# Performance work log

Measured on AMD Instinct MI355X. Metric: run time of the kernel, lower is better.

## Reference

```python
import jax, jax.numpy as jnp
import numpy as np

# dims: batch, tokens, channels, heads, head_dim, slices, context_slices, context_dim
B, N, C, H, D, G, SC, DC = 2, 32768, 256, 8, 32, 32, 64, 32
EPS_SLICE = 1e-5


def _ln(x, g, b):
    m = x.mean(-1, keepdims=True)
    v = ((x - m) ** 2).mean(-1, keepdims=True)
    return (x - m) * jax.lax.rsqrt(v + 1e-5) * g + b


def setup_inputs() -> dict:
    key = jax.random.key(0)
    ks = jax.random.split(key, 16)
    w = lambda k, s: jax.random.normal(k, s, jnp.float32) * 0.02
    return dict(
        fx=jax.random.normal(ks[0], (B, N, C), jnp.float32),
        context=jax.random.normal(ks[1], (B, H, SC, DC), jnp.float32),
        ln1_g=jnp.ones((C,), jnp.float32), ln1_b=jnp.zeros((C,), jnp.float32),
        Wfx=w(ks[2], (C, H * D)), bfx=jnp.zeros((H * D,), jnp.float32),
        Wx=w(ks[3], (C, H * D)), bx=jnp.zeros((H * D,), jnp.float32),
        Wslice=w(ks[4], (D, G)), bslice=jnp.zeros((G,), jnp.float32),
        temperature=0.5 * jnp.ones((1, H, 1, 1), jnp.float32),
        Wq=w(ks[5], (D, D)), Wk=w(ks[6], (D, D)), Wv=w(ks[7], (D, D)),
        Wcq=w(ks[8], (D, D)), bcq=jnp.zeros((D,), jnp.float32),
        Wck=w(ks[9], (DC, D)), bck=jnp.zeros((D,), jnp.float32),
        Wcv=w(ks[10], (DC, D)), bcv=jnp.zeros((D,), jnp.float32),
        state_mixing=jnp.zeros((), jnp.float32),
        Wout=w(ks[11], (H * D, C)), bout=jnp.zeros((C,), jnp.float32),
        ln2_g=jnp.ones((C,), jnp.float32), ln2_b=jnp.zeros((C,), jnp.float32),
        Wm1=w(ks[12], (C, 4 * C)), bm1=jnp.zeros((4 * C,), jnp.float32),
        Wm2=w(ks[13], (4 * C, C)), bm2=jnp.zeros((C,), jnp.float32),
    )


def reference(fx, context, ln1_g, ln1_b, Wfx, bfx, Wx, bx, Wslice, bslice,
              temperature, Wq, Wk, Wv, Wcq, bcq, Wck, bck, Wcv, bcv,
              state_mixing, Wout, bout, ln2_g, ln2_b, Wm1, bm1, Wm2, bm2):
    # --- GALE attention on pre-normed input (Transolver physics attention + cross) ---
    x = _ln(fx, ln1_g, ln1_b)
    fxm = (x @ Wfx + bfx).reshape(B, N, H, D).transpose(0, 2, 1, 3)  # b h n d
    xm = (x @ Wx + bx).reshape(B, N, H, D).transpose(0, 2, 1, 3)    # b h n d
    # slice weights: softmax over slices with learnable per-head temperature
    sw = jax.nn.softmax((xm @ Wslice + bslice) / temperature, axis=-1)  # b h n g
    norm = sw.sum(2)  # b h g
    st = jnp.einsum('bhnd,bhng->bhgd', fxm, sw) / (norm + EPS_SLICE)[..., None]
    scale = D ** -0.5
    # self-attention among slice tokens (no bias on q/k/v)
    q, k, v = st @ Wq, st @ Wk, st @ Wv
    sattn = jax.nn.softmax(jnp.einsum('bhgd,bhmd->bhgm', q, k) * scale, axis=-1)
    self_tok = jnp.einsum('bhgm,bhmd->bhgd', sattn, v)
    # cross-attention of slice tokens onto geometry/global context
    cq = st @ Wcq + bcq
    ck = context @ Wck + bck
    cv = context @ Wcv + bcv
    cattn = jax.nn.softmax(jnp.einsum('bhgd,bhsd->bhgs', cq, ck) * scale, axis=-1)
    cross_tok = jnp.einsum('bhgs,bhsd->bhgd', cattn, cv)
    # sigmoid-gated mix
    mw = jax.nn.sigmoid(state_mixing)
    ost = mw * self_tok + (1.0 - mw) * cross_tok
    # de-slice back to tokens and output-project
    out = jnp.einsum('bhgd,bhng->bhnd', ost, sw)
    out = out.transpose(0, 2, 1, 3).reshape(B, N, H * D) @ Wout + bout
    fx = fx + out  # residual 1
    # --- MLP block ---
    h = _ln(fx, ln2_g, ln2_b)
    fx = fx + (jax.nn.gelu(h @ Wm1 + bm1, approximate=False) @ Wm2 + bm2)
    return fx
```

## Files before the change

### kernel.cpp

```cpp
#include <hip/hip_runtime.h>
#include <hip/hip_bf16.h>

#define BATCH 2
#define NTOK  32768
#define CH    256
#define NH    8
#define HDIM  32
#define NG    32
#define NSC   64
#define NDC   32

typedef __attribute__((ext_vector_type(8))) short short8v;
typedef __attribute__((ext_vector_type(4))) short short4v;
typedef __attribute__((ext_vector_type(4))) float f32x4;

static __device__ __forceinline__ short f2bf(float f) {
    __hip_bfloat16 h = __float2bfloat16(f);
    return __builtin_bit_cast(short, h);
}
static __device__ __forceinline__ float bf2f(short s) {
    return __bfloat162float(__builtin_bit_cast(__hip_bfloat16, s));
}

__global__ __launch_bounds__(256) void kconv_transpose(
    const float* __restrict__ in, __hip_bfloat16* __restrict__ out,
    int K, int N)
{
    __shared__ float t[32][33];
    const int nb = N >> 5;
    const int bk = blockIdx.x / nb;
    const int bn = blockIdx.x % nb;
    const int c = threadIdx.x & 31, r0 = threadIdx.x >> 5;
    #pragma unroll
    for (int i = 0; i < 4; ++i) {
        const int r = r0 + i * 8;
        t[r][c] = in[(long)(bk * 32 + r) * N + bn * 32 + c];
    }
    __syncthreads();
    #pragma unroll
    for (int i = 0; i < 4; ++i) {
        const int r = r0 + i * 8;
        out[(long)(bn * 32 + r) * K + bk * 32 + c] = __float2bfloat16(t[c][r]);
    }
}

__global__ __launch_bounds__(256) void kcomb(
    const float* __restrict__ Wx, const float* __restrict__ bx,
    const float* __restrict__ Wsl, const float* __restrict__ bsl,
    __hip_bfloat16* __restrict__ wcat2, float* __restrict__ bcomb)
{
    __shared__ float wcol[32];
    const int hc = blockIdx.x;
    const int h = hc >> 5, g = hc & 31;
    const int tid = threadIdx.x;
    if (tid < 32) wcol[tid] = Wsl[tid * 32 + g];
    __syncthreads();
    float a = 0.f;
    #pragma unroll
    for (int d = 0; d < 32; ++d) a += Wx[tid * 256 + h * 32 + d] * wcol[d];
    wcat2[(long)hc * 256 + tid] = __float2bfloat16(a);
    if (tid == 0) {
        float s = bsl[g];
        #pragma unroll
        for (int d = 0; d < 32; ++d) s += bx[h * 32 + d] * wcol[d];
        bcomb[hc] = s;
    }
}

__global__ __launch_bounds__(256, 2) void k1_mfma(
    const float* __restrict__ fx,
    const float* __restrict__ g1, const float* __restrict__ b1,
    const __hip_bfloat16* __restrict__ wcat,
    const float* __restrict__ bfx, const float* __restrict__ bcomb,
    const float* __restrict__ temp,
    __hip_bfloat16* __restrict__ fxm_o, __hip_bfloat16* __restrict__ sw_o)
{
    __shared__ __align__(16) char lds[65536];
    const int tid = threadIdx.x;
    const int lane = tid & 63, wid = tid >> 6;
    const long tok0 = (long)blockIdx.x * 64;
    const int col = lane & 15, kq = lane >> 4;
    const int swz = (col & 7) << 4;
    const int ep = ((kq * 16) ^ swz) & 48;
    const int e0 = (swz & 64) | ep;
    const int e1 = ((swz & 64) ^ 64) | ep;
    const int ab0 = col * 512 + e0, ab1 = col * 512 + e1;

    {
        const float4 gv = *reinterpret_cast<const float4*>(g1 + lane * 4);
        const float4 bv = *reinterpret_cast<const float4*>(b1 + lane * 4);
        for (int tt = 0; tt < 16; ++tt) {
            const int r = wid * 16 + tt;
            const float4 v = *reinterpret_cast<const float4*>(fx + (tok0 + r) * 256 + lane * 4);
            float s = v.x + v.y + v.z + v.w;
            float s2 = v.x * v.x + v.y * v.y + v.z * v.z + v.w * v.w;
            #pragma unroll
            for (int off = 32; off; off >>= 1) {
                s  += __shfl_xor(s,  off);
                s2 += __shfl_xor(s2, off);
            }
            const float mean = s * (1.f / 256.f);
            const float rs = rsqrtf(s2 * (1.f / 256.f) - mean * mean + 1e-5f);
            short4v o;
            o[0] = f2bf((v.x - mean) * rs * gv.x + bv.x);
            o[1] = f2bf((v.y - mean) * rs * gv.y + bv.y);
            o[2] = f2bf((v.z - mean) * rs * gv.z + bv.z);
            o[3] = f2bf((v.w - mean) * rs * gv.w + bv.w);
            const int addr = r * 512 + ((lane * 8) ^ ((r & 7) << 4));
            *reinterpret_cast<short4v*>(lds + addr) = o;
        }
    }
    __syncthreads();

    f32x4 acc[4][8];
    #pragma unroll
    for (int mt = 0; mt < 4; ++mt)
        #pragma unroll
        for (int nt = 0; nt < 8; ++nt) acc[mt][nt] = (f32x4){0.f, 0.f, 0.f, 0.f};

    const short* wp = reinterpret_cast<const short*>(wcat) + (wid * 128 + col) * 256 + kq * 8;
    #pragma unroll 2
    for (int j = 0; j < 4; ++j) {
        short8v a0[4], a1[4];
        #pragma unroll
        for (int mt = 0; mt < 4; ++mt) {
            a0[mt] = *reinterpret_cast<const short8v*>(lds + mt * 8192 + j * 128 + ab0);
            a1[mt] = *reinterpret_cast<const short8v*>(lds + mt * 8192 + j * 128 + ab1);
        }
        #pragma unroll
        for (int nt = 0; nt < 8; ++nt) {
            const short8v b0 = *reinterpret_cast<const short8v*>(wp + nt * 4096 + j * 64);
            const short8v b1 = *reinterpret_cast<const short8v*>(wp + nt * 4096 + j * 64 + 32);
            #pragma unroll
            for (int mt = 0; mt < 4; ++mt) {
                acc[mt][nt] = __builtin_amdgcn_mfma_f32_16x16x32_bf16(a0[mt], b0, acc[mt][nt], 0, 0, 0);
                acc[mt][nt] = __builtin_amdgcn_mfma_f32_16x16x32_bf16(a1[mt], b1, acc[mt][nt], 0, 0, 0);
            }
        }
    }
    __syncthreads();

    #pragma unroll
    for (int nt = 0; nt < 8; ++nt) {
        const int c = wid * 128 + nt * 16 + col;
        const float bb = (c < 256) ? bfx[c] : bcomb[c - 256];
        #pragma unroll
        for (int mt = 0; mt < 4; ++mt) {
            #pragma unroll
            for (int r = 0; r < 4; ++r) {
                const int row = mt * 16 + kq * 4 + r;
                const int byte = row * 1024 + ((c * 2) ^ ((row & 7) << 4));
                *reinterpret_cast<short*>(lds + byte) = f2bf(acc[mt][nt][r] + bb);
            }
        }
    }
    __syncthreads();

    #pragma unroll
    for (int it = 0; it < 8; ++it) {
        const int idx = it * 256 + tid;
        const int row = idx >> 5, ch = idx & 31;
        const short8v val = *reinterpret_cast<const short8v*>(
            lds + row * 1024 + ((ch * 16) ^ ((row & 7) << 4)));
        *reinterpret_cast<short8v*>(
            reinterpret_cast<short*>(fxm_o) + (tok0 + row) * 256 + ch * 8) = val;
    }

    #pragma unroll
    for (int pp = 0; pp < 2; ++pp) {
        const int p = pp * 256 + tid;
        const int t = p >> 3, h = p & 7;
        const float it_ = 1.f / temp[h];
        float lg[32];
        #pragma unroll
        for (int g = 0; g < 32; ++g) {
            const int byte = t * 1024 + (((256 + h * 32 + g) * 2) ^ ((t & 7) << 4));
            lg[g] = bf2f(*reinterpret_cast<const short*>(lds + byte)) * it_;
        }
        float mx = -1e30f;
        #pragma unroll
        for (int g = 0; g < 32; ++g) mx = fmaxf(mx, lg[g]);
        float ssum = 0.f;
        #pragma unroll
        for (int g = 0; g < 32; ++g) { lg[g] = __expf(lg[g] - mx); ssum += lg[g]; }
        const float inv = 1.f / ssum;
        #pragma unroll
        for (int g = 0; g < 32; ++g) {
            const int byte = t * 1024 + (((256 + h * 32 + g) * 2) ^ ((t & 7) << 4));
            *reinterpret_cast<short*>(lds + byte) = f2bf(lg[g] * inv);
        }
    }
    __syncthreads();

    #pragma unroll
    for (int it = 0; it < 8; ++it) {
        const int idx = it * 256 + tid;
        const int row = idx >> 5, ch = idx & 31;
        const short8v val = *reinterpret_cast<const short8v*>(
            lds + row * 1024 + ((512 + ch * 16) ^ ((row & 7) << 4)));
        *reinterpret_cast<short8v*>(
            reinterpret_cast<short*>(sw_o) + (tok0 + row) * 256 + ch * 8) = val;
    }
}

__global__ __launch_bounds__(256) void k2_st_partial(
    const __hip_bfloat16* __restrict__ fxm, const __hip_bfloat16* __restrict__ sw,
    float* __restrict__ pst, float* __restrict__ pn)
{
    __shared__ float psum[4][32][32];
    __shared__ float pns[4][32];
    const int tid = threadIdx.x, wid = tid >> 6, lane = tid & 63;
    const int blk = blockIdx.x;
    const int bh = blk >> 5, chunk = blk & 31;
    const int b = bh >> 3, h = bh & 7;
    const long rbase = (long)b * NTOK + (long)chunk * 1024 + wid * 256;
    const int gB = lane >> 3, dB = lane & 7;
    const short* sp = reinterpret_cast<const short*>(sw) + rbase * 256 + h * 32 + gB * 4;
    const short* fp = reinterpret_cast<const short*>(fxm) + rbase * 256 + h * 32 + dB * 4;

    float acc[4][4];
    float nacc[4];
    #pragma unroll
    for (int i = 0; i < 4; ++i) {
        nacc[i] = 0.f;
        #pragma unroll
        for (int j = 0; j < 4; ++j) acc[i][j] = 0.f;
    }

    #pragma unroll 4
    for (int r = 0; r < 256; ++r) {
        const short4v s4 = *reinterpret_cast<const short4v*>(sp + r * 256);
        const short4v f4 = *reinterpret_cast<const short4v*>(fp + r * 256);
        float sg[4], fd[4];
        #pragma unroll
        for (int i = 0; i < 4; ++i) { sg[i] = bf2f(s4[i]); fd[i] = bf2f(f4[i]); }
        #pragma unroll
        for (int gg = 0; gg < 4; ++gg) {
            nacc[gg] += sg[gg];
            #pragma unroll
            for (int dd = 0; dd < 4; ++dd) acc[gg][dd] += sg[gg] * fd[dd];
        }
    }

    #pragma unroll
    for (int gg = 0; gg < 4; ++gg) {
        #pragma unroll
        for (int dd = 0; dd < 4; ++dd)
            psum[wid][gB * 4 + gg][dB * 4 + dd] = acc[gg][dd];
        if (dB == 0) pns[wid][gB * 4 + gg] = nacc[gg];
    }
    __syncthreads();

    for (int i = tid; i < 1024; i += 256) {
        const int g = i >> 5, d = i & 31;
        pst[(long)blk * 1024 + i] =
            psum[0][g][d] + psum[1][g][d] + psum[2][g][d] + psum[3][g][d];
    }
    if (tid < 32)
        pn[blk * 32 + tid] = pns[0][tid] + pns[1][tid] + pns[2][tid] + pns[3][tid];
}

__global__ __launch_bounds__(256) void k3_slice_attn(
    const float* __restrict__ pst, const float* __restrict__ pn,
    const float* __restrict__ ctx,
    const float* __restrict__ Wq, const float* __restrict__ Wk, const float* __restrict__ Wv,
    const float* __restrict__ Wcq, const float* __restrict__ bcq,
    const float* __restrict__ Wck, const float* __restrict__ bck,
    const float* __restrict__ Wcv, const float* __restrict__ bcv,
    const float* __restrict__ mix, __hip_bfloat16* __restrict__ ostT_o)
{
    __shared__ float st[1024], qm[1024], km[1024], vm[1024], cqm[1024];
    __shared__ float ckm[2048], cvm[2048], attn[2048], stok[1024], nb[32];
    const int tid = threadIdx.x;
    const int bh = blockIdx.x;

    if (tid < 32) {
        float s = 0.f;
        for (int c = 0; c < 32; ++c) s += pn[(bh * 32 + c) * 32 + tid];
        nb[tid] = s;
    }
    __syncthreads();
    for (int i = tid; i < 1024; i += 256) {
        float s = 0.f;
        for (int c = 0; c < 32; ++c) s += pst[(long)(bh * 32 + c) * 1024 + i];
        st[i] = s / (nb[i >> 5] + 1e-5f);
    }
    __syncthreads();

    for (int i = tid; i < 1024; i += 256) {
        const int g = i >> 5, d = i & 31;
        float aq = 0.f, ak = 0.f, av = 0.f, ac = bcq[d];
        #pragma unroll
        for (int e = 0; e < 32; ++e) {
            const float s = st[g * 32 + e];
            aq += s * Wq[e * 32 + d];
            ak += s * Wk[e * 32 + d];
            av += s * Wv[e * 32 + d];
            ac += s * Wcq[e * 32 + d];
        }
        qm[i] = aq; km[i] = ak; vm[i] = av; cqm[i] = ac;
    }
    const float* cbp = ctx + (long)bh * (NSC * NDC);
    for (int i = tid; i < 2048; i += 256) {
        const int s_ = i >> 5, d = i & 31;
        float w1 = bck[d], w2 = bcv[d];
        #pragma unroll
        for (int e = 0; e < 32; ++e) {
            const float cval = cbp[s_ * 32 + e];
            w1 += cval * Wck[e * 32 + d];
            w2 += cval * Wcv[e * 32 + d];
        }
        ckm[i] = w1; cvm[i] = w2;
    }
    __syncthreads();

    const float scale = 0.17677669529663687f;
    for (int i = tid; i < 1024; i += 256) {
        const int g = i >> 5, m = i & 31;
        float a = 0.f;
        #pragma unroll
        for (int d = 0; d < 32; ++d) a += qm[g * 32 + d] * km[m * 32 + d];
        attn[i] = a * scale;
    }
    __syncthreads();
    if (tid < 32) {
        float mx = -1e30f;
        for (int m = 0; m < 32; ++m) mx = fmaxf(mx, attn[tid * 32 + m]);
        float s = 0.f;
        for (int m = 0; m < 32; ++m) { const float e = expf(attn[tid * 32 + m] - mx); attn[tid * 32 + m] = e; s += e; }
        const float inv = 1.f / s;
        for (int m = 0; m < 32; ++m) attn[tid * 32 + m] *= inv;
    }
    __syncthreads();
    for (int i = tid; i < 1024; i += 256) {
        const int g = i >> 5, d = i & 31;
        float a = 0.f;
        #pragma unroll
        for (int m = 0; m < 32; ++m) a += attn[g * 32 + m] * vm[m * 32 + d];
        stok[i] = a;
    }
    __syncthreads();
    for (int i = tid; i < 2048; i += 256) {
        const int g = i >> 6, s_ = i & 63;
        float a = 0.f;
        #pragma unroll
        for (int d = 0; d < 32; ++d) a += cqm[g * 32 + d] * ckm[s_ * 32 + d];
        attn[i] = a * scale;
    }
    __syncthreads();
    if (tid < 32) {
        float mx = -1e30f;
        for (int m = 0; m < 64; ++m) mx = fmaxf(mx, attn[tid * 64 + m]);
        float s = 0.f;
        for (int m = 0; m < 64; ++m) { const float e = expf(attn[tid * 64 + m] - mx); attn[tid * 64 + m] = e; s += e; }
        const float inv = 1.f / s;
        for (int m = 0; m < 64; ++m) attn[tid * 64 + m] *= inv;
    }
    __syncthreads();
    const float mw = 1.f / (1.f + expf(-mix[0]));
    for (int i = tid; i < 1024; i += 256) {
        const int g = i >> 5, d = i & 31;
        float a = 0.f;
        #pragma unroll
        for (int s_ = 0; s_ < 64; ++s_) a += attn[g * 64 + s_] * cvm[s_ * 32 + d];
        const float val = mw * stok[i] + (1.f - mw) * a;
        ostT_o[(long)bh * 1024 + d * 32 + g] = __float2bfloat16(val);
    }
}

__global__ __launch_bounds__(256, 2) void k4_mfma(
    const __hip_bfloat16* __restrict__ sw, const __hip_bfloat16* __restrict__ ostT,
    const __hip_bfloat16* __restrict__ woutt, const float* __restrict__ bout,
    const float* __restrict__ fx, float* __restrict__ out)
{
    __shared__ __align__(16) char lds[65536];
    const int tid = threadIdx.x;
    const int lane = tid & 63, wid = tid >> 6;
    const long tok0 = (long)blockIdx.x * 64;
    const int b = (int)(tok0 >> 15);
    const int col = lane & 15, kq = lane >> 4;
    const int swz = (col & 7) << 4;
    const int ep = ((kq * 16) ^ swz) & 48;
    const int e0 = (swz & 64) | ep;
    const int e1 = ((swz & 64) ^ 64) | ep;
    const int ab0 = col * 512 + e0, ab1 = col * 512 + e1;

    #pragma unroll
    for (int it = 0; it < 8; ++it) {
        const int idx = it * 256 + tid;
        const int row = idx >> 5, ch = idx & 31;
        const short8v val = *reinterpret_cast<const short8v*>(
            reinterpret_cast<const short*>(sw) + (tok0 + row) * 256 + ch * 8);
        *reinterpret_cast<short8v*>(lds + row * 512 + ((ch * 16) ^ ((row & 7) << 4))) = val;
    }
    __syncthreads();

    f32x4 accal[2][4][2];
    #pragma unroll
    for (int hh = 0; hh < 2; ++hh) {
        const int h = wid * 2 + hh;
        short8v a[4];
        #pragma unroll
        for (int mt = 0; mt < 4; ++mt)
            a[mt] = *reinterpret_cast<const short8v*>(
                lds + mt * 8192 + wid * 128 + (hh ? ab1 : ab0));
        #pragma unroll
        for (int nt = 0; nt < 2; ++nt) {
            const int d = nt * 16 + col;
            const short8v bfr = *reinterpret_cast<const short8v*>(
                reinterpret_cast<const short*>(ostT) + ((b * 8 + h) * 32 + d) * 32 + kq * 8);
            #pragma unroll
            for (int mt = 0; mt < 4; ++mt) {
                accal[hh][mt][nt] = (f32x4){0.f, 0.f, 0.f, 0.f};
                accal[hh][mt][nt] = __builtin_amdgcn_mfma_f32_16x16x32_bf16(
                    a[mt], bfr, accal[hh][mt][nt], 0, 0, 0);
            }
        }
    }
    #pragma unroll
    for (int hh = 0; hh < 2; ++hh) {
        const int h = wid * 2 + hh;
        #pragma unroll
        for (int nt = 0; nt < 2; ++nt) {
            const int cc = h * 32 + nt * 16 + col;
            #pragma unroll
            for (int mt = 0; mt < 4; ++mt) {
                #pragma unroll
                for (int r = 0; r < 4; ++r) {
                    const int row = mt * 16 + kq * 4 + r;
                    const int byte = 32768 + row * 512 + ((cc * 2) ^ ((row & 7) << 4));
                    *reinterpret_cast<short*>(lds + byte) = f2bf(accal[hh][mt][nt][r]);
                }
            }
        }
    }
    __syncthreads();

    f32x4 acc[4][4];
    #pragma unroll
    for (int mt = 0; mt < 4; ++mt)
        #pragma unroll
        for (int nt = 0; nt < 4; ++nt) acc[mt][nt] = (f32x4){0.f, 0.f, 0.f, 0.f};

    const short* wp = reinterpret_cast<const short*>(woutt) + (wid * 64 + col) * 256 + kq * 8;
    #pragma unroll 2
    for (int j = 0; j < 4; ++j) {
        short8v a0[4], a1[4];
        #pragma unroll
        for (int mt = 0; mt < 4; ++mt) {
            a0[mt] = *reinterpret_cast<const short8v*>(lds + 32768 + mt * 8192 + j * 128 + ab0);
            a1[mt] = *reinterpret_cast<const short8v*>(lds + 32768 + mt * 8192 + j * 128 + ab1);
        }
        #pragma unroll
        for (int nt = 0; nt < 4; ++nt) {
            const short8v b0 = *reinterpret_cast<const short8v*>(wp + nt * 4096 + j * 64);
            const short8v b1 = *reinterpret_cast<const short8v*>(wp + nt * 4096 + j * 64 + 32);
            #pragma unroll
            for (int mt = 0; mt < 4; ++mt) {
                acc[mt][nt] = __builtin_amdgcn_mfma_f32_16x16x32_bf16(a0[mt], b0, acc[mt][nt], 0, 0, 0);
                acc[mt][nt] = __builtin_amdgcn_mfma_f32_16x16x32_bf16(a1[mt], b1, acc[mt][nt], 0, 0, 0);
            }
        }
    }

    __syncthreads();
    float* lf = reinterpret_cast<float*>(lds);
    #pragma unroll
    for (int nt = 0; nt < 4; ++nt) {
        const int c = wid * 64 + nt * 16 + col;
        const float bb = bout[c];
        #pragma unroll
        for (int mt = 0; mt < 4; ++mt) {
            #pragma unroll
            for (int r = 0; r < 4; ++r) {
                const int row = mt * 16 + kq * 4 + r;
                lf[row * 256 + c] = acc[mt][nt][r] + bb;
            }
        }
    }
    __syncthreads();
    #pragma unroll
    for (int it = 0; it < 16; ++it) {
        const int q = it * 256 + tid;
        const int row = q >> 6, c4 = (q & 63) * 4;
        const float4 v = *reinterpret_cast<const float4*>(lf + row * 256 + c4);
        const long gidx = (tok0 + row) * 256 + c4;
        const float4 f = *reinterpret_cast<const float4*>(fx + gidx);
        float4 o;
        o.x = v.x + f.x; o.y = v.y + f.y; o.z = v.z + f.z; o.w = v.w + f.w;
        *reinterpret_cast<float4*>(out + gidx) = o;
    }
}

__global__ __launch_bounds__(512, 4) void k5_mlp_mfma(
    float* __restrict__ io,
    const float* __restrict__ g2, const float* __restrict__ b2,
    const __hip_bfloat16* __restrict__ w1t, const float* __restrict__ bm1,
    const __hip_bfloat16* __restrict__ w2t, const float* __restrict__ bm2)
{
    __shared__ __align__(16) char lds[49152];
    const int tid = threadIdx.x;
    const int lane = tid & 63, wid = tid >> 6;
    const long tok0 = (long)blockIdx.x * 64;
    const int col = lane & 15, kq = lane >> 4;
    const int n0 = wid * 32;
    const int h0 = wid * 16;
    const int swz = (col & 7) << 4;
    const int ep = ((kq * 16) ^ swz) & 48;
    const int e0 = (swz & 64) | ep;
    const int e1 = ((swz & 64) ^ 64) | ep;
    const int ab0 = col * 512 + e0, ab1 = col * 512 + e1;
    const int cb0 = col * 256 + e0, cb1 = col * 256 + e1;

    {
        const float4 gv = *reinterpret_cast<const float4*>(g2 + lane * 4);
        const float4 bv = *reinterpret_cast<const float4*>(b2 + lane * 4);
        #pragma unroll
        for (int tt = 0; tt < 8; ++tt) {
            const int r = wid * 8 + tt;
            const float4 v = *reinterpret_cast<const float4*>(io + (tok0 + r) * 256 + lane * 4);
            float s = v.x + v.y + v.z + v.w;
            float s2 = v.x * v.x + v.y * v.y + v.z * v.z + v.w * v.w;
            #pragma unroll
            for (int off = 32; off; off >>= 1) {
                s  += __shfl_xor(s,  off);
                s2 += __shfl_xor(s2, off);
            }
            const float mean = s * (1.f / 256.f);
            const float rs = rsqrtf(s2 * (1.f / 256.f) - mean * mean + 1e-5f);
            short4v o;
            o[0] = f2bf((v.x - mean) * rs * gv.x + bv.x);
            o[1] = f2bf((v.y - mean) * rs * gv.y + bv.y);
            o[2] = f2bf((v.z - mean) * rs * gv.z + bv.z);
            o[3] = f2bf((v.w - mean) * rs * gv.w + bv.w);
            const int addr = r * 512 + ((lane * 8) ^ ((r & 7) << 4));
            *reinterpret_cast<short4v*>(lds + addr) = o;
        }
    }
    __syncthreads();

    const short* w1s = reinterpret_cast<const short*>(w1t) + (h0 + col) * 256 + kq * 8;
    const short* w2s = reinterpret_cast<const short*>(w2t) + (n0 + col) * 1024 + kq * 8;

    f32x4 accO[4][2];
    #pragma unroll
    for (int mt = 0; mt < 4; ++mt)
        #pragma unroll
        for (int nt = 0; nt < 2; ++nt) accO[mt][nt] = (f32x4){0.f, 0.f, 0.f, 0.f};

    for (int ch = 0; ch < 8; ++ch) {
        f32x4 accP[4];
        #pragma unroll
        for (int mt = 0; mt < 4; ++mt) accP[mt] = (f32x4){0.f, 0.f, 0.f, 0.f};

        #pragma unroll 1
        for (int j = 0; j < 4; ++j) {
            const short8v b0 = *reinterpret_cast<const short8v*>(w1s + ch * 32768 + j * 64);
            const short8v b1 = *reinterpret_cast<const short8v*>(w1s + ch * 32768 + j * 64 + 32);
            #pragma unroll
            for (int mt = 0; mt < 4; ++mt) {
                const short8v a0 = *reinterpret_cast<const short8v*>(lds + mt * 8192 + j * 128 + ab0);
                const short8v a1 = *reinterpret_cast<const short8v*>(lds + mt * 8192 + j * 128 + ab1);
                accP[mt] = __builtin_amdgcn_mfma_f32_16x16x32_bf16(a0, b0, accP[mt], 0, 0, 0);
                accP[mt] = __builtin_amdgcn_mfma_f32_16x16x32_bf16(a1, b1, accP[mt], 0, 0, 0);
            }
        }

        __syncthreads();
        {
            const float b1v = bm1[ch * 128 + h0 + col];
            const int k2i2 = (h0 + col) * 2;
            #pragma unroll
            for (int mt = 0; mt < 4; ++mt) {
                #pragma unroll
                for (int r = 0; r < 4; ++r) {
                    float m = accP[mt][r] + b1v;
                    const float u = __builtin_fmaf(0.044715f * m, m * m, m);
                    const float e = __expf(-1.5957691216057308f * u);
                    m = m * __builtin_amdgcn_rcpf(1.f + e);
                    const int row = mt * 16 + kq * 4 + r;
                    const int byte = 32768 + row * 256 + (k2i2 ^ ((row & 7) << 4));
                    *reinterpret_cast<short*>(lds + byte) = f2bf(m);
                }
            }
        }
        __syncthreads();

        #pragma unroll 1
        for (int j = 0; j < 2; ++j) {
            short8v b20[2], b21[2];
            #pragma unroll
            for (int nt = 0; nt < 2; ++nt) {
                b20[nt] = *reinterpret_cast<const short8v*>(w2s + nt * 16384 + ch * 128 + j * 64);
                b21[nt] = *reinterpret_cast<const short8v*>(w2s + nt * 16384 + ch * 128 + j * 64 + 32);
            }
            #pragma unroll
            for (int mt = 0; mt < 4; ++mt) {
                const short8v x0 = *reinterpret_cast<const short8v*>(lds + 32768 + mt * 4096 + j * 128 + cb0);
                const short8v x1 = *reinterpret_cast<const short8v*>(lds + 32768 + mt * 4096 + j * 128 + cb1);
                #pragma unroll
                for (int nt = 0; nt < 2; ++nt) {
                    accO[mt][nt] = __builtin_amdgcn_mfma_f32_16x16x32_bf16(x0, b20[nt], accO[mt][nt], 0, 0, 0);
                    accO[mt][nt] = __builtin_amdgcn_mfma_f32_16x16x32_bf16(x1, b21[nt], accO[mt][nt], 0, 0, 0);
                }
            }
        }
    }

    __syncthreads();
    float* lf = reinterpret_cast<float*>(lds);
    #pragma unroll
    for (int half = 0; half < 2; ++half) {
        if ((wid >> 2) == half) {
            #pragma unroll
            for (int nt = 0; nt < 2; ++nt) {
                const int c = n0 + nt * 16 + col;
                const float b2v = bm2[c];
                const int cl = c - half * 128;
                #pragma unroll
                for (int mt = 0; mt < 4; ++mt) {
                    #pragma unroll
                    for (int r = 0; r < 4; ++r) {
                        const int row = mt * 16 + kq * 4 + r;
                        lf[row * 128 + cl] = accO[mt][nt][r] + b2v;
                    }
                }
            }
        }
        __syncthreads();
        #pragma unroll
        for (int it = 0; it < 4; ++it) {
            const int q = it * 512 + tid;
            const int row = q >> 5, c4 = (q & 31) * 4;
            const float4 v = *reinterpret_cast<const float4*>(lf + row * 128 + c4);
            const long gidx = (tok0 + row) * 256 + half * 128 + c4;
            const float4 f = *reinterpret_cast<const float4*>(io + gidx);
            float4 o;
            o.x = v.x + f.x; o.y = v.y + f.y; o.z = v.z + f.z; o.w = v.w + f.w;
            *reinterpret_cast<float4*>(io + gidx) = o;
        }
        __syncthreads();
    }
}

extern "C" void kernel_launch(void* const* d_in, const int* in_sizes, int n_in,
                              void* d_out, int out_size, void* d_ws, size_t ws_size,
                              hipStream_t stream)
{
    const float* fx   = (const float*)d_in[0];
    const float* ctx  = (const float*)d_in[1];
    const float* g1   = (const float*)d_in[2];
    const float* b1   = (const float*)d_in[3];
    const float* Wfx  = (const float*)d_in[4];
    const float* bfx  = (const float*)d_in[5];
    const float* Wx   = (const float*)d_in[6];
    const float* bx   = (const float*)d_in[7];
    const float* Wsl  = (const float*)d_in[8];
    const float* bsl  = (const float*)d_in[9];
    const float* temp = (const float*)d_in[10];
    const float* Wq   = (const float*)d_in[11];
    const float* Wk   = (const float*)d_in[12];
    const float* Wv   = (const float*)d_in[13];
    const float* Wcq  = (const float*)d_in[14];
    const float* bcq  = (const float*)d_in[15];
    const float* Wck  = (const float*)d_in[16];
    const float* bck  = (const float*)d_in[17];
    const float* Wcv  = (const float*)d_in[18];
    const float* bcv  = (const float*)d_in[19];
    const float* mix  = (const float*)d_in[20];
    const float* Wout = (const float*)d_in[21];
    const float* bout = (const float*)d_in[22];
    const float* g2   = (const float*)d_in[23];
    const float* b2   = (const float*)d_in[24];
    const float* Wm1  = (const float*)d_in[25];
    const float* bm1  = (const float*)d_in[26];
    const float* Wm2  = (const float*)d_in[27];
    const float* bm2  = (const float*)d_in[28];
    float* out = (float*)d_out;

    char* ws = (char*)d_ws;
    __hip_bfloat16* fxm  = (__hip_bfloat16*)ws;
    __hip_bfloat16* sw   = (__hip_bfloat16*)(ws + (size_t)33554432);
    float* pst = (float*)(ws + (size_t)67108864);
    float* pn  = (float*)(ws + (size_t)69206016);
    __hip_bfloat16* ostT  = (__hip_bfloat16*)(ws + (size_t)69271552);
    __hip_bfloat16* wcat  = (__hip_bfloat16*)(ws + (size_t)69304320);
    __hip_bfloat16* woutt = (__hip_bfloat16*)(ws + (size_t)69566464);
    __hip_bfloat16* w1t   = (__hip_bfloat16*)(ws + (size_t)69697536);
    __hip_bfloat16* w2t   = (__hip_bfloat16*)(ws + (size_t)70221824);
    float* bcomb          = (float*)(ws + (size_t)70746112);

    kconv_transpose<<<64,  256, 0, stream>>>(Wfx, wcat,  256, 256);
    kcomb<<<256, 256, 0, stream>>>(Wx, bx, Wsl, bsl, wcat + 65536, bcomb);
    kconv_transpose<<<64,  256, 0, stream>>>(Wout, woutt, 256, 256);
    kconv_transpose<<<256, 256, 0, stream>>>(Wm1, w1t,    256, 1024);
    kconv_transpose<<<256, 256, 0, stream>>>(Wm2, w2t,    1024, 256);

    k1_mfma<<<1024, 256, 0, stream>>>(fx, g1, b1, wcat, bfx, bcomb, temp,
                                      fxm, sw);
    k2_st_partial<<<512, 256, 0, stream>>>(fxm, sw, pst, pn);
    k3_slice_attn<<<16, 256, 0, stream>>>(pst, pn, ctx, Wq, Wk, Wv,
                                          Wcq, bcq, Wck, bck, Wcv, bcv, mix, ostT);
    k4_mfma<<<1024, 256, 0, stream>>>(sw, ostT, woutt, bout, fx, out);
    k5_mlp_mfma<<<1024, 512, 0, stream>>>(out, g2, b2, w1t, bm1, w2t, bm2);
}
```

Measured before the change: 324.9 us.

## Fuse de-slice/output-projection kernel with MLP block into one kernel

Merges the de-slice plus Wout projection kernel and the LN2+MLP kernel into a single 512-thread kernel. The residual-1 result stays in registers and LDS instead of being written to global memory and read back. The work is remapped so each of 8 waves handles one head and a 32-column slice of the output. The two MLP inner loops are also unrolled by 2. In exchange, each thread holds more registers and the kernel uses 64KB of LDS, which may limit occupancy below the requested 4 blocks per SM.

```diff
diff --git a/kernel.cpp b/kernel.cpp
--- a/kernel.cpp
+++ b/kernel.cpp
@@ -368,10 +368,14 @@
     }
 }
 
-__global__ __launch_bounds__(256, 2) void k4_mfma(
+__global__ __launch_bounds__(512, 4) void k45_fused(
     const __hip_bfloat16* __restrict__ sw, const __hip_bfloat16* __restrict__ ostT,
     const __hip_bfloat16* __restrict__ woutt, const float* __restrict__ bout,
-    const float* __restrict__ fx, float* __restrict__ out)
+    const float* __restrict__ fx,
+    const float* __restrict__ g2, const float* __restrict__ b2,
+    const __hip_bfloat16* __restrict__ w1t, const float* __restrict__ bm1,
+    const __hip_bfloat16* __restrict__ w2t, const float* __restrict__ bm2,
+    float* __restrict__ out)
 {
     __shared__ __align__(16) char lds[65536];
     const int tid = threadIdx.x;
@@ -384,10 +388,11 @@
     const int e0 = (swz & 64) | ep;
     const int e1 = ((swz & 64) ^ 64) | ep;
     const int ab0 = col * 512 + e0, ab1 = col * 512 + e1;
-
-    #pragma unroll
-    for (int it = 0; it < 8; ++it) {
-        const int idx = it * 256 + tid;
+    const int cb0 = col * 256 + e0, cb1 = col * 256 + e1;
+
+    #pragma unroll
+    for (int it = 0; it < 4; ++it) {
+        const int idx = it * 512 + tid;
         const int row = idx >> 5, ch = idx & 31;
         const short8v val = *reinterpret_cast<const short8v*>(
             reinterpret_cast<const short*>(sw) + (tok0 + row) * 256 + ch * 8);
@@ -395,70 +400,66 @@
     }
     __syncthreads();
 
-    f32x4 accal[2][4][2];
-    #pragma unroll
-    for (int hh = 0; hh < 2; ++hh) {
-        const int h = wid * 2 + hh;
+    {
+        f32x4 accal[4][2];
+        const int abh = col * 512 + (((wid * 64) | (kq * 16)) ^ swz);
         short8v a[4];
         #pragma unroll
         for (int mt = 0; mt < 4; ++mt)
-            a[mt] = *reinterpret_cast<const short8v*>(
-                lds + mt * 8192 + wid * 128 + (hh ? ab1 : ab0));
+            a[mt] = *reinterpret_cast<const short8v*>(lds + mt * 8192 + abh);
         #pragma unroll
         for (int nt = 0; nt < 2; ++nt) {
             const int d = nt * 16 + col;
             const short8v bfr = *reinterpret_cast<const short8v*>(
-                reinterpret_cast<const short*>(ostT) + ((b * 8 + h) * 32 + d) * 32 + kq * 8);
+                reinterpret_cast<const short*>(ostT) + ((b * 8 + wid) * 32 + d) * 32 + kq * 8);
             #pragma unroll
             for (int mt = 0; mt < 4; ++mt) {
-                accal[hh][mt][nt] = (f32x4){0.f, 0.f, 0.f, 0.f};
-                accal[hh][mt][nt] = __builtin_amdgcn_mfma_f32_16x16x32_bf16(
-                    a[mt], bfr, accal[hh][mt][nt], 0, 0, 0);
-            }
-        }
-    }
-    #pragma unroll
-    for (int hh = 0; hh < 2; ++hh) {
-        const int h = wid * 2 + hh;
+                accal[mt][nt] = (f32x4){0.f, 0.f, 0.f, 0.f};
+                accal[mt][nt] = __builtin_amdgcn_mfma_f32_16x16x32_bf16(
+                    a[mt], bfr, accal[mt][nt], 0, 0, 0);
+            }
+        }
         #pragma unroll
         for (int nt = 0; nt < 2; ++nt) {
-            const int cc = h * 32 + nt * 16 + col;
+            const int cc = wid * 32 + nt * 16 + col;
             #pragma unroll
             for (int mt = 0; mt < 4; ++mt) {
                 #pragma unroll
                 for (int r = 0; r < 4; ++r) {
                     const int row = mt * 16 + kq * 4 + r;
                     const int byte = 32768 + row * 512 + ((cc * 2) ^ ((row & 7) << 4));
-                    *reinterpret_cast<short*>(lds + byte) = f2bf(accal[hh][mt][nt][r]);
+                    *reinterpret_cast<short*>(lds + byte) = f2bf(accal[mt][nt][r]);
                 }
             }
         }
     }
     __syncthreads();
 
-    f32x4 acc[4][4];
+    f32x4 acc[4][2];
     #pragma unroll
     for (int mt = 0; mt < 4; ++mt)
         #pragma unroll
-        for (int nt = 0; nt < 4; ++nt) acc[mt][nt] = (f32x4){0.f, 0.f, 0.f, 0.f};
-
-    const short* wp = reinterpret_cast<const short*>(woutt) + (wid * 64 + col) * 256 + kq * 8;
-    #pragma unroll 2
-    for (int j = 0; j < 4; ++j) {
-        short8v a0[4], a1[4];
-        #pragma unroll
-        for (int mt = 0; mt < 4; ++mt) {
-            a0[mt] = *reinterpret_cast<const short8v*>(lds + 32768 + mt * 8192 + j * 128 + ab0);
-            a1[mt] = *reinterpret_cast<const short8v*>(lds + 32768 + mt * 8192 + j * 128 + ab1);
-        }
-        #pragma unroll
-        for (int nt = 0; nt < 4; ++nt) {
-            const short8v b0 = *reinterpret_cast<const short8v*>(wp + nt * 4096 + j * 64);
-            const short8v b1 = *reinterpret_cast<const short8v*>(wp + nt * 4096 + j * 64 + 32);
+        for (int nt = 0; nt < 2; ++nt) acc[mt][nt] = (f32x4){0.f, 0.f, 0.f, 0.f};
+
+    {
+        const short* wp = reinterpret_cast<const short*>(woutt) + (wid * 32 + col) * 256 + kq * 8;
+        #pragma unroll 2
+        for (int j = 0; j < 4; ++j) {
+            short8v a0[4], a1[4];
             #pragma unroll
             for (int mt = 0; mt < 4; ++mt) {
-                acc[mt][nt] = __builtin_amdgcn_mfma_f32_16x16x32_bf16(a0[mt], b0, acc[mt][nt], 0, 0, 0);
-                acc[mt][nt] = __builtin_amdgcn_mfma_f32_16x16x32_bf16(a1[mt], b1, acc[mt][nt], 0, 0, 0);
+                a0[mt] = *reinterpret_cast<const short8v*>(lds + 32768 + mt * 8192 + j * 128 + ab0);
+                a1[mt] = *reinterpret_cast<const short8v*>(lds + 32768 + mt * 8192 + j * 128 + ab1);
+            }
+            #pragma unroll
+            for (int nt = 0; nt < 2; ++nt) {
+                const short8v b0 = *reinterpret_cast<const short8v*>(wp + nt * 4096 + j * 64);
+                const short8v b1 = *reinterpret_cast<const short8v*>(wp + nt * 4096 + j * 64 + 32);
+                #pragma unroll
+                for (int mt = 0; mt < 4; ++mt) {
+                    acc[mt][nt] = __builtin_amdgcn_mfma_f32_16x16x32_bf16(a0[mt], b0, acc[mt][nt], 0, 0, 0);
+                    acc[mt][nt] = __builtin_amdgcn_mfma_f32_16x16x32_bf16(a1[mt], b1, acc[mt][nt], 0, 0, 0);
+                }
             }
         }
     }
@@ -466,8 +467,8 @@
     __syncthreads();
     float* lf = reinterpret_cast<float*>(lds);
     #pragma unroll
-    for (int nt = 0; nt < 4; ++nt) {
-        const int c = wid * 64 + nt * 16 + col;
+    for (int nt = 0; nt < 2; ++nt) {
+        const int c = wid * 32 + nt * 16 + col;
         const float bb = bout[c];
         #pragma unroll
         for (int mt = 0; mt < 4; ++mt) {
@@ -479,48 +480,22 @@
         }
     }
     __syncthreads();
-    #pragma unroll
-    for (int it = 0; it < 16; ++it) {
-        const int q = it * 256 + tid;
-        const int row = q >> 6, c4 = (q & 63) * 4;
-        const float4 v = *reinterpret_cast<const float4*>(lf + row * 256 + c4);
-        const long gidx = (tok0 + row) * 256 + c4;
-        const float4 f = *reinterpret_cast<const float4*>(fx + gidx);
-        float4 o;
-        o.x = v.x + f.x; o.y = v.y + f.y; o.z = v.z + f.z; o.w = v.w + f.w;
-        *reinterpret_cast<float4*>(out + gidx) = o;
-    }
-}
-
-__global__ __launch_bounds__(512, 4) void k5_mlp_mfma(
-    float* __restrict__ io,
-    const float* __restrict__ g2, const float* __restrict__ b2,
-    const __hip_bfloat16* __restrict__ w1t, const float* __restrict__ bm1,
-    const __hip_bfloat16* __restrict__ w2t, const float* __restrict__ bm2)
-{
-    __shared__ __align__(16) char lds[49152];
-    const int tid = threadIdx.x;
-    const int lane = tid & 63, wid = tid >> 6;
-    const long tok0 = (long)blockIdx.x * 64;
-    const int col = lane & 15, kq = lane >> 4;
-    const int n0 = wid * 32;
-    const int h0 = wid * 16;
-    const int swz = (col & 7) << 4;
-    const int ep = ((kq * 16) ^ swz) & 48;
-    const int e0 = (swz & 64) | ep;
-    const int e1 = ((swz & 64) ^ 64) | ep;
-    const int ab0 = col * 512 + e0, ab1 = col * 512 + e1;
-    const int cb0 = col * 256 + e0, cb1 = col * 256 + e1;
-
+
+    f32x4 oa[8];
+    short4v aout[8];
     {
         const float4 gv = *reinterpret_cast<const float4*>(g2 + lane * 4);
         const float4 bv = *reinterpret_cast<const float4*>(b2 + lane * 4);
         #pragma unroll
         for (int tt = 0; tt < 8; ++tt) {
             const int r = wid * 8 + tt;
-            const float4 v = *reinterpret_cast<const float4*>(io + (tok0 + r) * 256 + lane * 4);
-            float s = v.x + v.y + v.z + v.w;
-            float s2 = v.x * v.x + v.y * v.y + v.z * v.z + v.w * v.w;
+            const float4 l4 = *reinterpret_cast<const float4*>(lf + r * 256 + lane * 4);
+            const float4 f4 = *reinterpret_cast<const float4*>(fx + (tok0 + r) * 256 + lane * 4);
+            const float vx = l4.x + f4.x, vy = l4.y + f4.y;
+            const float vz = l4.z + f4.z, vw = l4.w + f4.w;
+            oa[tt] = (f32x4){vx, vy, vz, vw};
+            float s = vx + vy + vz + vw;
+            float s2 = vx * vx + vy * vy + vz * vz + vw * vw;
             #pragma unroll
             for (int off = 32; off; off >>= 1) {
                 s  += __shfl_xor(s,  off);
@@ -528,17 +503,23 @@
             }
             const float mean = s * (1.f / 256.f);
             const float rs = rsqrtf(s2 * (1.f / 256.f) - mean * mean + 1e-5f);
-            short4v o;
-            o[0] = f2bf((v.x - mean) * rs * gv.x + bv.x);
-            o[1] = f2bf((v.y - mean) * rs * gv.y + bv.y);
-            o[2] = f2bf((v.z - mean) * rs * gv.z + bv.z);
-            o[3] = f2bf((v.w - mean) * rs * gv.w + bv.w);
-            const int addr = r * 512 + ((lane * 8) ^ ((r & 7) << 4));
-            *reinterpret_cast<short4v*>(lds + addr) = o;
-        }
-    }
-    __syncthreads();
-
+            aout[tt][0] = f2bf((vx - mean) * rs * gv.x + bv.x);
+            aout[tt][1] = f2bf((vy - mean) * rs * gv.y + bv.y);
+            aout[tt][2] = f2bf((vz - mean) * rs * gv.z + bv.z);
+            aout[tt][3] = f2bf((vw - mean) * rs * gv.w + bv.w);
+        }
+    }
+    __syncthreads();
+    #pragma unroll
+    for (int tt = 0; tt < 8; ++tt) {
+        const int r = wid * 8 + tt;
+        const int addr = r * 512 + ((lane * 8) ^ ((r & 7) << 4));
+        *reinterpret_cast<short4v*>(lds + addr) = aout[tt];
+    }
+    __syncthreads();
+
+    const int n0 = wid * 32;
+    const int h0 = wid * 16;
     const short* w1s = reinterpret_cast<const short*>(w1t) + (h0 + col) * 256 + kq * 8;
     const short* w2s = reinterpret_cast<const short*>(w2t) + (n0 + col) * 1024 + kq * 8;
 
@@ -553,7 +534,7 @@
         #pragma unroll
         for (int mt = 0; mt < 4; ++mt) accP[mt] = (f32x4){0.f, 0.f, 0.f, 0.f};
 
-        #pragma unroll 1
+        #pragma unroll 2
         for (int j = 0; j < 4; ++j) {
             const short8v b0 = *reinterpret_cast<const short8v*>(w1s + ch * 32768 + j * 64);
             const short8v b1 = *reinterpret_cast<const short8v*>(w1s + ch * 32768 + j * 64 + 32);
@@ -586,7 +567,7 @@
         }
         __syncthreads();
 
-        #pragma unroll 1
+        #pragma unroll 2
         for (int j = 0; j < 2; ++j) {
             short8v b20[2], b21[2];
             #pragma unroll
@@ -608,38 +589,30 @@
     }
 
     __syncthreads();
-    float* lf = reinterpret_cast<float*>(lds);
-    #pragma unroll
-    for (int half = 0; half < 2; ++half) {
-        if ((wid >> 2) == half) {
-            #pragma unroll
-            for (int nt = 0; nt < 2; ++nt) {
-                const int c = n0 + nt * 16 + col;
-                const float b2v = bm2[c];
-                const int cl = c - half * 128;
-                #pragma unroll
-                for (int mt = 0; mt < 4; ++mt) {
-                    #pragma unroll
-                    for (int r = 0; r < 4; ++r) {
-                        const int row = mt * 16 + kq * 4 + r;
-                        lf[row * 128 + cl] = accO[mt][nt][r] + b2v;
-                    }
-                }
-            }
-        }
-        __syncthreads();
-        #pragma unroll
-        for (int it = 0; it < 4; ++it) {
-            const int q = it * 512 + tid;
-            const int row = q >> 5, c4 = (q & 31) * 4;
-            const float4 v = *reinterpret_cast<const float4*>(lf + row * 128 + c4);
-            const long gidx = (tok0 + row) * 256 + half * 128 + c4;
-            const float4 f = *reinterpret_cast<const float4*>(io + gidx);
-            float4 o;
-            o.x = v.x + f.x; o.y = v.y + f.y; o.z = v.z + f.z; o.w = v.w + f.w;
-            *reinterpret_cast<float4*>(io + gidx) = o;
-        }
-        __syncthreads();
+    #pragma unroll
+    for (int nt = 0; nt < 2; ++nt) {
+        const int c = n0 + nt * 16 + col;
+        const float b2v = bm2[c];
+        #pragma unroll
+        for (int mt = 0; mt < 4; ++mt) {
+            #pragma unroll
+            for (int r = 0; r < 4; ++r) {
+                const int row = mt * 16 + kq * 4 + r;
+                lf[row * 256 + c] = accO[mt][nt][r] + b2v;
+            }
+        }
+    }
+    __syncthreads();
+    #pragma unroll
+    for (int tt = 0; tt < 8; ++tt) {
+        const int r = wid * 8 + tt;
+        const float4 m4 = *reinterpret_cast<const float4*>(lf + r * 256 + lane * 4);
+        float4 o;
+        o.x = oa[tt][0] + m4.x;
+        o.y = oa[tt][1] + m4.y;
+        o.z = oa[tt][2] + m4.z;
+        o.w = oa[tt][3] + m4.w;
+        *reinterpret_cast<float4*>(out + (tok0 + r) * 256 + lane * 4) = o;
     }
 }
 
@@ -701,6 +674,6 @@
     k2_st_partial<<<512, 256, 0, stream>>>(fxm, sw, pst, pn);
     k3_slice_attn<<<16, 256, 0, stream>>>(pst, pn, ctx, Wq, Wk, Wv,
                                           Wcq, bcq, Wck, bck, Wcv, bcv, mix, ostT);
-    k4_mfma<<<1024, 256, 0, stream>>>(sw, ostT, woutt, bout, fx, out);
-    k5_mlp_mfma<<<1024, 512, 0, stream>>>(out, g2, b2, w1t, bm1, w2t, bm2);
-}
+    k45_fused<<<1024, 512, 0, stream>>>(sw, ostT, woutt, bout, fx,
+                                        g2, b2, w1t, bm1, w2t, bm2, out);
+}
```

Result: no change. 329.3 us (+1.4%).
